# Kernel optimization log

Measured on AMD Instinct MI355X. Metric: run time of the kernel, lower is better.

The kernel has to match this reference:

```python
import jax, jax.numpy as jnp
import numpy as np

N = 20000      # nodes
E = 320000     # edges
F = 128        # feat_dim
N_RBF = 20
CUTOFF = 5.0


def setup_inputs() -> dict:
    key = jax.random.key(0)
    ks = jax.random.split(key, 12)
    h_i = jax.random.normal(ks[0], (N, F), dtype=jnp.float32)
    v_i = jax.random.normal(ks[1], (N, F, 3), dtype=jnp.float32)
    # distances in (0, cutoff); keep strictly > 0 to avoid div-by-zero in sinc basis
    d_ij = (jax.random.uniform(ks[2], (E,), dtype=jnp.float32) * 0.98 + 0.01) * CUTOFF
    r = jax.random.normal(ks[3], (E, 3), dtype=jnp.float32)
    unit_r_ij = r / jnp.linalg.norm(r, axis=-1, keepdims=True)
    nbrs = jax.random.randint(ks[4], (E, 2), 0, N, dtype=jnp.int64)
    # params: layers = Dense(F->F, swish) then Dense(F->3F); dist_embed dense: n_rbf -> 3F
    s1 = 1.0 / np.sqrt(F)
    W1 = jax.random.uniform(ks[5], (F, F), jnp.float32, -s1, s1)
    b1 = jax.random.uniform(ks[6], (F,), jnp.float32, -s1, s1)
    W2 = jax.random.uniform(ks[7], (F, 3 * F), jnp.float32, -s1, s1)
    b2 = jax.random.uniform(ks[8], (3 * F,), jnp.float32, -s1, s1)
    sr = 1.0 / np.sqrt(N_RBF)
    Wr = jax.random.uniform(ks[9], (N_RBF, 3 * F), jnp.float32, -sr, sr)
    br = jax.random.uniform(ks[10], (3 * F,), jnp.float32, -sr, sr)
    return {"h_i": h_i, "v_i": v_i, "d_ij": d_ij, "unit_r_ij": unit_r_ij,
            "nbrs": nbrs, "W1": W1, "b1": b1, "W2": W2, "b2": b2, "Wr": Wr, "br": br}


def _dist_embed(d, Wr, br):
    # PaiNN sinc-like radial basis: sin(n*pi*d/cutoff)/d, n=1..N_RBF
    n = jnp.arange(1, N_RBF + 1, dtype=d.dtype)
    rbf = jnp.sin(n[None, :] * jnp.pi * d[:, None] / CUTOFF) / d[:, None]  # [E, N_RBF]
    # cosine cutoff envelope
    fcut = 0.5 * (jnp.cos(jnp.pi * d / CUTOFF) + 1.0) * (d < CUTOFF)       # [E]
    return (rbf @ Wr + br) * fcut[:, None]                                  # [E, 3F]


def reference(h_i, v_i, d_ij, unit_r_ij, nbrs, W1, b1, W2, b2, Wr, br):
    # phi = Dense(swish) -> Dense : [N, 3F]
    phi = jax.nn.silu(h_i @ W1 + b1) @ W2 + b2
    src = nbrs[:, 1]
    dst = nbrs[:, 0]
    edge_inv = phi[src] * _dist_embed(d_ij, Wr, br)          # [E, 3F]
    edge_inv = edge_inv.reshape(edge_inv.shape[0], 3, F)     # [E, 3, F]
    f1, f2, f3 = edge_inv[:, 0], edge_inv[:, 1], edge_inv[:, 2]
    # dv: [E, F, 3]
    dv = f1[:, :, None] * unit_r_ij[:, None, :] + f2[:, :, None] * v_i[src]
    dh_i = jax.ops.segment_sum(f3, dst, num_segments=N)      # [N, F]
    dv_i = jax.ops.segment_sum(dv, dst, num_segments=N)      # [N, F, 3]
    return (dh_i, dv_i)
```

## Files before the change

### kernel.cpp

```cpp
#include <hip/hip_runtime.h>
#include <math.h>

#define F 128
#define THREEF 384
#define N_RBF 20
#define CUTOFF 5.0f
#define CAP 64
#define TLDS_STRIDE 136

typedef __bf16 bf16x8 __attribute__((ext_vector_type(8)));
typedef float  f32x4  __attribute__((ext_vector_type(4)));
typedef float  f32x2  __attribute__((ext_vector_type(2)));

__global__ __launch_bounds__(256) void init_kernel(
    const float* __restrict__ W1, const float* __restrict__ W2,
    const float* __restrict__ Wr,
    __bf16* __restrict__ W1T, __bf16* __restrict__ W2T,
    float* __restrict__ WrT, int* __restrict__ cnt, int N)
{
    const int tid = threadIdx.x;
    const int b   = blockIdx.x;

    if (b < 256) {
        const int idx = b * 256 + tid;
        if (idx < 128 * 128) {
            const int n = idx >> 7, k = idx & 127;
            W1T[idx] = (__bf16)W1[k * F + n];
        }
        if (idx < 384 * 128) {
            const int n = idx >> 7, k = idx & 127;
            W2T[idx] = (__bf16)W2[k * THREEF + n];
        }
    } else if (b < 264) {
        const int idx = (b - 256) * 256 + tid;
        if (idx >= 5 * 3 * 128) return;
        const int f  = idx & 127;
        const int c  = (idx >> 7) % 3;
        const int n4 = idx / (3 * 128);
        float4 v;
        v.x = Wr[(4 * n4 + 0) * THREEF + c * 128 + f];
        v.y = Wr[(4 * n4 + 1) * THREEF + c * 128 + f];
        v.z = Wr[(4 * n4 + 2) * THREEF + c * 128 + f];
        v.w = Wr[(4 * n4 + 3) * THREEF + c * 128 + f];
        ((float4*)WrT)[idx] = v;
    } else {
        const int i = (b - 264) * 256 + tid;
        if (i < (N + 3) / 4) {
            int4 z; z.x = 0; z.y = 0; z.z = 0; z.w = 0;
            ((int4*)cnt)[i] = z;
        }
    }
}

__global__ __launch_bounds__(256) void work_kernel(
    const float* __restrict__ d_ij, const float* __restrict__ unit_r,
    const int* __restrict__ nbrs,
    int* __restrict__ cnt, float* __restrict__ pack,
    const float* __restrict__ h,
    const __bf16* __restrict__ W1T, const float* __restrict__ b1,
    const __bf16* __restrict__ W2T, const float* __restrict__ b2,
    float* __restrict__ phi, int E, int EB, int N)
{
    __shared__ __bf16 t_lds[16 * TLDS_STRIDE];

    const int tid = threadIdx.x;
    const int b   = blockIdx.x;

    if (b < EB) {
        const int e = b * 256 + tid;
        if (e >= E) return;
        const int2 nb = ((const int2*)nbrs)[e];
        const int dst = nb.x;
        const int src = nb.y;
        const int slot = atomicAdd(&cnt[dst], 1);
        if (slot >= CAP) return;

        const float d = d_ij[e];
        const float x = (float)M_PI * d * (1.0f / CUTOFF);
        float sx, cx;
        __sincosf(x, &sx, &cx);
        const float fcut = (d < CUTOFF) ? 0.5f * (cx + 1.0f) : 0.0f;
        float4 q0, q1;
        q0.x = sx * fcut / d;
        q0.y = 2.0f * cx;
        q0.z = fcut;
        q0.w = unit_r[3 * e + 0];
        q1.x = unit_r[3 * e + 1];
        q1.y = unit_r[3 * e + 2];
        q1.z = __int_as_float(src);
        q1.w = 0.0f;
        float4* pk = (float4*)(pack + ((size_t)dst * CAP + slot) * 8);
        pk[0] = q0;
        pk[1] = q1;
        return;
    }

    const int wave = tid >> 6;
    const int lane = tid & 63;
    const int m    = lane & 15;
    const int quad = lane >> 4;
    const int node0 = (b - EB) * 16;
    if (node0 >= N) return;

    bf16x8 a1[4];
    #pragma unroll
    for (int kb = 0; kb < 4; ++kb) {
        const float* hp = h + (size_t)(node0 + m) * F + kb * 32 + quad * 8;
        const float4 x0 = *(const float4*)hp;
        const float4 x1 = *(const float4*)(hp + 4);
        bf16x8 a;
        a[0] = (__bf16)x0.x; a[1] = (__bf16)x0.y;
        a[2] = (__bf16)x0.z; a[3] = (__bf16)x0.w;
        a[4] = (__bf16)x1.x; a[5] = (__bf16)x1.y;
        a[6] = (__bf16)x1.z; a[7] = (__bf16)x1.w;
        a1[kb] = a;
    }

    #pragma unroll
    for (int c2 = 0; c2 < 2; ++c2) {
        const int ct = wave * 2 + c2;
        f32x4 acc = {0.0f, 0.0f, 0.0f, 0.0f};
        #pragma unroll
        for (int kb = 0; kb < 4; ++kb) {
            const bf16x8 bb =
                *(const bf16x8*)(W1T + (size_t)(ct * 16 + m) * F + kb * 32 + quad * 8);
            acc = __builtin_amdgcn_mfma_f32_16x16x32_bf16(a1[kb], bb, acc, 0, 0, 0);
        }
        const int col = ct * 16 + m;
        const float bb = b1[col];
        #pragma unroll
        for (int reg = 0; reg < 4; ++reg) {
            const float x = acc[reg] + bb;
            const float s = x / (1.0f + __expf(-x));
            t_lds[(quad * 4 + reg) * TLDS_STRIDE + col] = (__bf16)s;
        }
    }
    __syncthreads();

    bf16x8 a2[4];
    #pragma unroll
    for (int kb = 0; kb < 4; ++kb)
        a2[kb] = *(const bf16x8*)&t_lds[m * TLDS_STRIDE + kb * 32 + quad * 8];

    #pragma unroll
    for (int c6 = 0; c6 < 6; ++c6) {
        const int ct = c6 * 4 + wave;
        f32x4 acc = {0.0f, 0.0f, 0.0f, 0.0f};
        #pragma unroll
        for (int kb = 0; kb < 4; ++kb) {
            const bf16x8 bb =
                *(const bf16x8*)(W2T + (size_t)(ct * 16 + m) * F + kb * 32 + quad * 8);
            acc = __builtin_amdgcn_mfma_f32_16x16x32_bf16(a2[kb], bb, acc, 0, 0, 0);
        }
        const int col   = ct * 16 + m;
        const int plane = col >> 7;
        const int fc    = col & 127;
        const float bb  = b2[col];
        float* pp = phi + (size_t)plane * N * F + fc;
        #pragma unroll
        for (int reg = 0; reg < 4; ++reg) {
            const int row = quad * 4 + reg;
            pp[(size_t)(node0 + row) * F] = acc[reg] + bb;
        }
    }
}

__global__ __launch_bounds__(256) void gather_kernel(
    const float* __restrict__ phi,
    const float* __restrict__ v_i,
    const float* __restrict__ WrT,
    const float* __restrict__ br,
    const int*   __restrict__ cnt,
    const float* __restrict__ pack,
    float* __restrict__ dh,
    float* __restrict__ dv,
    int N)
{
    __shared__ float4 s_pack[2][CAP * 2];

    const int tid  = threadIdx.x;
    const int half = tid >> 7;
    const int f    = tid & 127;
    const int node = blockIdx.x * 2 + half;

    const int deg0 = cnt[node];
    const int deg  = deg0 < CAP ? deg0 : CAP;

    {
        const float4* src = (const float4*)(pack + (size_t)node * CAP * 8);
        if (f < 2 * deg) s_pack[half][f] = src[f];
    }
    __syncthreads();

    const float br0 = br[f], br1 = br[f + 128], br2 = br[f + 256];

    const float* phi0 = phi;
    const float* phi1 = phi + (size_t)N * F;
    const float* phi2 = phi + (size_t)2 * N * F;
    const f32x4* wT   = (const f32x4*)WrT;

    float dh_acc = 0.0f, dv0 = 0.0f, dv1 = 0.0f, dv2 = 0.0f;

    for (int i = 0; i < deg; ++i) {
        const float* q = (const float*)&s_pack[half][2 * i];
        const float s1   = q[0];
        const float twoc = q[1];
        const float fcut = q[2];
        const float ux   = q[3];
        const float uy   = q[4];
        const float uz   = q[5];
        const int src = __builtin_amdgcn_readfirstlane(__float_as_int(q[6]));

        const float t2s = fmaf(twoc, twoc, -2.0f);
        f32x2 t2; t2[0] = t2s;  t2[1] = t2s;
        f32x2 rc; rc[0] = s1;   rc[1] = twoc * s1;
        f32x2 rp; rp[0] = -s1;  rp[1] = 0.0f;
        f32x2 A0 = {0.0f, 0.0f}, A1 = {0.0f, 0.0f}, A2 = {0.0f, 0.0f};

        #pragma unroll
        for (int n4 = 0; n4 < 5; ++n4) {
            const f32x4 w0 = wT[(n4 * 3 + 0) * 128 + f];
            const f32x4 w1 = wT[(n4 * 3 + 1) * 128 + f];
            const f32x4 w2 = wT[(n4 * 3 + 2) * 128 + f];
            A0 = __builtin_elementwise_fma(rc, __builtin_shufflevector(w0, w0, 0, 1), A0);
            A1 = __builtin_elementwise_fma(rc, __builtin_shufflevector(w1, w1, 0, 1), A1);
            A2 = __builtin_elementwise_fma(rc, __builtin_shufflevector(w2, w2, 0, 1), A2);
            f32x2 rn = __builtin_elementwise_fma(t2, rc, -rp);
            rp = rc; rc = rn;
            A0 = __builtin_elementwise_fma(rc, __builtin_shufflevector(w0, w0, 2, 3), A0);
            A1 = __builtin_elementwise_fma(rc, __builtin_shufflevector(w1, w1, 2, 3), A1);
            A2 = __builtin_elementwise_fma(rc, __builtin_shufflevector(w2, w2, 2, 3), A2);
            rn = __builtin_elementwise_fma(t2, rc, -rp);
            rp = rc; rc = rn;
        }

        const float a0 = fmaf(br0, fcut, A0[0] + A0[1]);
        const float a1 = fmaf(br1, fcut, A1[0] + A1[1]);
        const float a2 = fmaf(br2, fcut, A2[0] + A2[1]);

        const float f1 = phi0[(size_t)src * F + f] * a0;
        const float f2 = phi1[(size_t)src * F + f] * a1;
        const float f3 = phi2[(size_t)src * F + f] * a2;

        dh_acc += f3;

        const float* vs = v_i + (size_t)src * THREEF + 3 * f;
        dv0 = fmaf(f1, ux, fmaf(f2, vs[0], dv0));
        dv1 = fmaf(f1, uy, fmaf(f2, vs[1], dv1));
        dv2 = fmaf(f1, uz, fmaf(f2, vs[2], dv2));
    }

    dh[(size_t)node * F + f] = dh_acc;
    float* dvp = dv + (size_t)node * THREEF + 3 * f;
    dvp[0] = dv0;
    dvp[1] = dv1;
    dvp[2] = dv2;
}

extern "C" void kernel_launch(void* const* d_in, const int* in_sizes, int n_in,
                              void* d_out, int out_size, void* d_ws, size_t ws_size,
                              hipStream_t stream) {
    const float* h_i    = (const float*)d_in[0];
    const float* v_i    = (const float*)d_in[1];
    const float* d_ij   = (const float*)d_in[2];
    const float* unit_r = (const float*)d_in[3];
    const int*   nbrs   = (const int*)  d_in[4];
    const float* W1     = (const float*)d_in[5];
    const float* b1     = (const float*)d_in[6];
    const float* W2     = (const float*)d_in[7];
    const float* b2     = (const float*)d_in[8];
    const float* Wr     = (const float*)d_in[9];
    const float* br     = (const float*)d_in[10];

    const int N = in_sizes[0] / F;
    const int E = in_sizes[2];

    float* dh = (float*)d_out;
    float* dv = dh + (size_t)N * F;

    float*  phi  = (float*)d_ws;
    float*  pack = phi + (size_t)3 * N * F;
    float*  WrT  = pack + (size_t)N * CAP * 8;
    int*    cnt  = (int*)(WrT + 5 * 3 * 128 * 4);
    __bf16* W1T  = (__bf16*)(cnt + N);
    __bf16* W2T  = W1T + 128 * 128;

    const int EB = (E + 255) / 256;
    const int MB = (N + 15) / 16;
    const int ZB = ((N + 3) / 4 + 255) / 256;

    init_kernel<<<256 + 8 + ZB, 256, 0, stream>>>(W1, W2, Wr, W1T, W2T, WrT,
                                                  cnt, N);
    work_kernel<<<EB + MB, 256, 0, stream>>>(d_ij, unit_r, nbrs, cnt, pack,
                                             h_i, W1T, b1, W2T, b2, phi,
                                             E, EB, N);
    gather_kernel<<<N / 2, 256, 0, stream>>>(phi, v_i, WrT, br, cnt, pack,
                                             dh, dv, N);
}
```

Measured before the change: 286.2 us.

## Batch four edges per gather iteration and interleave phi into node-major rows

The gather loop now processes edges in groups of four. All phi and v_i loads for the group are issued up front, before the Chebyshev-style radial-basis recurrences run, so several independent gather loads are in flight and the loop-carried latency is hidden. Padding edges are zero-filled in shared memory, so fcut and s1 are zero and they add nothing. phi is now written node-major with stride 3F, so the three planes for a source node sit next to each other, and a waves-per-EU hint is added. The cost is higher register pressure, which may lower occupancy, plus wasted work on padded edges.

```diff
diff --git a/kernel.cpp b/kernel.cpp
--- a/kernel.cpp
+++ b/kernel.cpp
@@ -152,20 +152,19 @@
                 *(const bf16x8*)(W2T + (size_t)(ct * 16 + m) * F + kb * 32 + quad * 8);
             acc = __builtin_amdgcn_mfma_f32_16x16x32_bf16(a2[kb], bb, acc, 0, 0, 0);
         }
-        const int col   = ct * 16 + m;
-        const int plane = col >> 7;
-        const int fc    = col & 127;
-        const float bb  = b2[col];
-        float* pp = phi + (size_t)plane * N * F + fc;
+        const int col = ct * 16 + m;
+        const float bb = b2[col];
         #pragma unroll
         for (int reg = 0; reg < 4; ++reg) {
             const int row = quad * 4 + reg;
-            pp[(size_t)(node0 + row) * F] = acc[reg] + bb;
+            phi[(size_t)(node0 + row) * THREEF + col] = acc[reg] + bb;
         }
     }
 }
 
-__global__ __launch_bounds__(256) void gather_kernel(
+__global__ __launch_bounds__(256)
+__attribute__((amdgpu_waves_per_eu(2, 4)))
+void gather_kernel(
     const float* __restrict__ phi,
     const float* __restrict__ v_i,
     const float* __restrict__ WrT,
@@ -185,76 +184,97 @@
 
     const int deg0 = cnt[node];
     const int deg  = deg0 < CAP ? deg0 : CAP;
+    const int degR = (deg + 3) & ~3;
 
     {
-        const float4* src = (const float4*)(pack + (size_t)node * CAP * 8);
-        if (f < 2 * deg) s_pack[half][f] = src[f];
+        const float4* srcp = (const float4*)(pack + (size_t)node * CAP * 8);
+        if (f < 2 * degR) {
+            float4 v = make_float4(0.0f, 0.0f, 0.0f, 0.0f);
+            if (f < 2 * deg) v = srcp[f];
+            s_pack[half][f] = v;
+        }
     }
     __syncthreads();
 
     const float br0 = br[f], br1 = br[f + 128], br2 = br[f + 256];
-
-    const float* phi0 = phi;
-    const float* phi1 = phi + (size_t)N * F;
-    const float* phi2 = phi + (size_t)2 * N * F;
-    const f32x4* wT   = (const f32x4*)WrT;
-
-    float dh_acc = 0.0f, dv0 = 0.0f, dv1 = 0.0f, dv2 = 0.0f;
-
-    for (int i = 0; i < deg; ++i) {
-        const float* q = (const float*)&s_pack[half][2 * i];
-        const float s1   = q[0];
-        const float twoc = q[1];
-        const float fcut = q[2];
-        const float ux   = q[3];
-        const float uy   = q[4];
-        const float uz   = q[5];
-        const int src = __builtin_amdgcn_readfirstlane(__float_as_int(q[6]));
-
-        const float t2s = fmaf(twoc, twoc, -2.0f);
-        f32x2 t2; t2[0] = t2s;  t2[1] = t2s;
-        f32x2 rc; rc[0] = s1;   rc[1] = twoc * s1;
-        f32x2 rp; rp[0] = -s1;  rp[1] = 0.0f;
-        f32x2 A0 = {0.0f, 0.0f}, A1 = {0.0f, 0.0f}, A2 = {0.0f, 0.0f};
+    const f32x4* wT = (const f32x4*)WrT;
+
+    float dh_acc = 0.0f, dvx = 0.0f, dvy = 0.0f, dvz = 0.0f;
+
+    for (int i0 = 0; i0 < degR; i0 += 4) {
+        float s1[4], twoc[4], fcut[4], ux[4], uy[4], uz[4];
+        float ph0[4], ph1[4], ph2[4], vx[4], vy[4], vz[4];
+        #pragma unroll
+        for (int j = 0; j < 4; ++j) {
+            const float4 q0 = s_pack[half][2 * (i0 + j)];
+            const float4 q1 = s_pack[half][2 * (i0 + j) + 1];
+            s1[j] = q0.x; twoc[j] = q0.y; fcut[j] = q0.z;
+            ux[j] = q0.w; uy[j] = q1.x;   uz[j] = q1.y;
+            const int src = __builtin_amdgcn_readfirstlane(__float_as_int(q1.z));
+            const float* pp = phi + (size_t)src * THREEF + f;
+            ph0[j] = pp[0];  ph1[j] = pp[128]; ph2[j] = pp[256];
+            const float* vs = v_i + (size_t)src * THREEF + 3 * f;
+            vx[j] = vs[0];   vy[j] = vs[1];    vz[j] = vs[2];
+        }
+
+        f32x2 t2[4], rc[4], rp[4], A0[4], A1[4], A2[4];
+        #pragma unroll
+        for (int j = 0; j < 4; ++j) {
+            const float t2s = fmaf(twoc[j], twoc[j], -2.0f);
+            t2[j][0] = t2s;      t2[j][1] = t2s;
+            rc[j][0] = s1[j];    rc[j][1] = twoc[j] * s1[j];
+            rp[j][0] = -s1[j];   rp[j][1] = 0.0f;
+            A0[j] = (f32x2){0.0f, 0.0f};
+            A1[j] = (f32x2){0.0f, 0.0f};
+            A2[j] = (f32x2){0.0f, 0.0f};
+        }
 
         #pragma unroll
         for (int n4 = 0; n4 < 5; ++n4) {
             const f32x4 w0 = wT[(n4 * 3 + 0) * 128 + f];
             const f32x4 w1 = wT[(n4 * 3 + 1) * 128 + f];
             const f32x4 w2 = wT[(n4 * 3 + 2) * 128 + f];
-            A0 = __builtin_elementwise_fma(rc, __builtin_shufflevector(w0, w0, 0, 1), A0);
-            A1 = __builtin_elementwise_fma(rc, __builtin_shufflevector(w1, w1, 0, 1), A1);
-            A2 = __builtin_elementwise_fma(rc, __builtin_shufflevector(w2, w2, 0, 1), A2);
-            f32x2 rn = __builtin_elementwise_fma(t2, rc, -rp);
-            rp = rc; rc = rn;
-            A0 = __builtin_elementwise_fma(rc, __builtin_shufflevector(w0, w0, 2, 3), A0);
-            A1 = __builtin_elementwise_fma(rc, __builtin_shufflevector(w1, w1, 2, 3), A1);
-            A2 = __builtin_elementwise_fma(rc, __builtin_shufflevector(w2, w2, 2, 3), A2);
-            rn = __builtin_elementwise_fma(t2, rc, -rp);
-            rp = rc; rc = rn;
-        }
-
-        const float a0 = fmaf(br0, fcut, A0[0] + A0[1]);
-        const float a1 = fmaf(br1, fcut, A1[0] + A1[1]);
-        const float a2 = fmaf(br2, fcut, A2[0] + A2[1]);
-
-        const float f1 = phi0[(size_t)src * F + f] * a0;
-        const float f2 = phi1[(size_t)src * F + f] * a1;
-        const float f3 = phi2[(size_t)src * F + f] * a2;
-
-        dh_acc += f3;
-
-        const float* vs = v_i + (size_t)src * THREEF + 3 * f;
-        dv0 = fmaf(f1, ux, fmaf(f2, vs[0], dv0));
-        dv1 = fmaf(f1, uy, fmaf(f2, vs[1], dv1));
-        dv2 = fmaf(f1, uz, fmaf(f2, vs[2], dv2));
+            const f32x2 w0lo = __builtin_shufflevector(w0, w0, 0, 1);
+            const f32x2 w1lo = __builtin_shufflevector(w1, w1, 0, 1);
+            const f32x2 w2lo = __builtin_shufflevector(w2, w2, 0, 1);
+            const f32x2 w0hi = __builtin_shufflevector(w0, w0, 2, 3);
+            const f32x2 w1hi = __builtin_shufflevector(w1, w1, 2, 3);
+            const f32x2 w2hi = __builtin_shufflevector(w2, w2, 2, 3);
+            #pragma unroll
+            for (int j = 0; j < 4; ++j) {
+                A0[j] = __builtin_elementwise_fma(rc[j], w0lo, A0[j]);
+                A1[j] = __builtin_elementwise_fma(rc[j], w1lo, A1[j]);
+                A2[j] = __builtin_elementwise_fma(rc[j], w2lo, A2[j]);
+                f32x2 rn = __builtin_elementwise_fma(t2[j], rc[j], -rp[j]);
+                rp[j] = rc[j]; rc[j] = rn;
+                A0[j] = __builtin_elementwise_fma(rc[j], w0hi, A0[j]);
+                A1[j] = __builtin_elementwise_fma(rc[j], w1hi, A1[j]);
+                A2[j] = __builtin_elementwise_fma(rc[j], w2hi, A2[j]);
+                rn = __builtin_elementwise_fma(t2[j], rc[j], -rp[j]);
+                rp[j] = rc[j]; rc[j] = rn;
+            }
+        }
+
+        #pragma unroll
+        for (int j = 0; j < 4; ++j) {
+            const float a0 = fmaf(br0, fcut[j], A0[j][0] + A0[j][1]);
+            const float a1 = fmaf(br1, fcut[j], A1[j][0] + A1[j][1]);
+            const float a2 = fmaf(br2, fcut[j], A2[j][0] + A2[j][1]);
+            const float f1 = ph0[j] * a0;
+            const float f2 = ph1[j] * a1;
+            const float f3 = ph2[j] * a2;
+            dh_acc += f3;
+            dvx = fmaf(f1, ux[j], fmaf(f2, vx[j], dvx));
+            dvy = fmaf(f1, uy[j], fmaf(f2, vy[j], dvy));
+            dvz = fmaf(f1, uz[j], fmaf(f2, vz[j], dvz));
+        }
     }
 
     dh[(size_t)node * F + f] = dh_acc;
     float* dvp = dv + (size_t)node * THREEF + 3 * f;
-    dvp[0] = dv0;
-    dvp[1] = dv1;
-    dvp[2] = dv2;
+    dvp[0] = dvx;
+    dvp[1] = dvy;
+    dvp[2] = dvz;
 }
 
 extern "C" void kernel_launch(void* const* d_in, const int* in_sizes, int n_in,
```

After: 281.0 us. About the same (-1.8%).
